# Kernel optimization log

Hardware: AMD Instinct MI355X
Metric: run time of the kernel (lower is better)

## Reference

```python
import jax, jax.numpy as jnp
import numpy as np

# Standard bitsandbytes NF4 codebook (16 values)
NF4_CODE = jnp.array([
    -1.0, -0.6961928009986877, -0.5250730514526367, -0.39491748809814453,
    -0.28444138169288635, -0.18477343022823334, -0.09105003625154495, 0.0,
    0.07958029955625534, 0.16093020141124725, 0.24611230194568634,
    0.33791524171829224, 0.44070982933044434, 0.5626170039176941,
    0.7229568362236023, 1.0], dtype=jnp.float32)

BLOCKSIZE = 64
IN_FEATURES = 4096
OUT_FEATURES = 11008


def setup_inputs() -> dict:
    key = jax.random.key(0)
    k1, k2, k3, k4 = jax.random.split(key, 4)
    x = jax.random.normal(k1, (4, 2048, IN_FEATURES), dtype=jnp.float32)
    weight_q = jax.random.randint(k2, (OUT_FEATURES, IN_FEATURES), 0, 16, dtype=jnp.int32)
    absmax = jax.random.uniform(k3, (OUT_FEATURES, IN_FEATURES // BLOCKSIZE), dtype=jnp.float32)
    bias = jax.random.normal(k4, (OUT_FEATURES,), dtype=jnp.float32)
    return {"x": x, "weight_q": weight_q, "absmax": absmax, "bias": bias}


def reference(x, weight_q, absmax, bias):
    out_f, in_f = weight_q.shape
    # Blockwise NF4 dequantization: code lookup * per-block absmax scale
    w_code = NF4_CODE[weight_q]                                   # [O, I]
    w_blocks = w_code.reshape(out_f, in_f // BLOCKSIZE, BLOCKSIZE)
    w = (w_blocks * absmax[:, :, None]).reshape(out_f, in_f)      # [O, I]
    # Linear: y = x @ W^T + b
    y = jnp.einsum('bsi,oi->bso', x, w) + bias
    return y
```

## Files before the change

### kernel.cpp

```cpp
#include <hip/hip_runtime.h>
#include <hip/hip_bf16.h>
#include <stdint.h>

typedef __attribute__((ext_vector_type(8))) short short8;
typedef __attribute__((ext_vector_type(8))) unsigned short ushort8;
typedef __attribute__((ext_vector_type(4))) float f32x4;

#define K_DIM 4096
#define N_DIM 11008
#define M_DIM 8192
#define BM 256
#define BN 256
#define BK 64
#define TILES (K_DIM / BK)

__constant__ float c_nf4[16] = {
    -1.0f, -0.6961928009986877f, -0.5250730514526367f, -0.39491748809814453f,
    -0.28444138169288635f, -0.18477343022823334f, -0.09105003625154495f, 0.0f,
    0.07958029955625534f, 0.16093020141124725f, 0.24611230194568634f,
    0.33791524171829224f, 0.44070982933044434f, 0.5626170039176941f,
    0.7229568362236023f, 1.0f};

__device__ __forceinline__ unsigned short f2bf(float f) {
    uint32_t u = __float_as_uint(f);
    u += 0x7fffu + ((u >> 16) & 1u);
    return (unsigned short)(u >> 16);
}

__global__ __launch_bounds__(256) void nf4_dequant_w(const int* __restrict__ q,
                                                     const float* __restrict__ absmax,
                                                     unsigned short* __restrict__ w) {
    __shared__ float lut[16];
    if (threadIdx.x < 16) lut[threadIdx.x] = c_nf4[threadIdx.x];
    __syncthreads();
    size_t t = (size_t)blockIdx.x * 256 + threadIdx.x;
    const int4* q4 = (const int4*)q;
    int4 qa = q4[2 * t];
    int4 qb = q4[2 * t + 1];
    float s = absmax[t >> 3];
    ushort8 o;
    o[0] = f2bf(lut[qa.x & 15] * s);
    o[1] = f2bf(lut[qa.y & 15] * s);
    o[2] = f2bf(lut[qa.z & 15] * s);
    o[3] = f2bf(lut[qa.w & 15] * s);
    o[4] = f2bf(lut[qb.x & 15] * s);
    o[5] = f2bf(lut[qb.y & 15] * s);
    o[6] = f2bf(lut[qb.z & 15] * s);
    o[7] = f2bf(lut[qb.w & 15] * s);
    ((ushort8*)w)[t] = o;
}

__global__ __launch_bounds__(256) void x_to_bf16(const float* __restrict__ x,
                                                 unsigned short* __restrict__ xb) {
    size_t t = (size_t)blockIdx.x * 256 + threadIdx.x;
    const float4* x4 = (const float4*)x;
    float4 a = x4[2 * t];
    float4 b = x4[2 * t + 1];
    ushort8 o;
    o[0] = f2bf(a.x); o[1] = f2bf(a.y); o[2] = f2bf(a.z); o[3] = f2bf(a.w);
    o[4] = f2bf(b.x); o[5] = f2bf(b.y); o[6] = f2bf(b.z); o[7] = f2bf(b.w);
    ((ushort8*)xb)[t] = o;
}

#define STAGE_HALF(gbase, lds_half, row0, k0)                                 \
  do {                                                                        \
    _Pragma("unroll")                                                         \
    for (int _g = 0; _g < 2; ++_g) {                                          \
      const int _i = _g * 512 + tid;                        \
      const int _r = _i >> 3;                           \
      const int _c = (_i & 7) ^ (_r & 7);                   \
      __builtin_amdgcn_global_load_lds(                                       \
          (const __attribute__((address_space(1))) void*)((gbase) +           \
              (size_t)((row0) + _r) * K_DIM + (k0) + _c * 8),                 \
          (__attribute__((address_space(3))) void*)((lds_half) +              \
              (_g * 512 + wave * 64) * 8),                                    \
          16, 0, 0);                                                          \
    }                                                                         \
  } while (0)

#define DS_A4(dst, rbase, X)                                                  \
  dst[0] = *(const short8*)(Ah + ((rbase) +  0) * 64 + (roff ^ (X)));         \
  dst[1] = *(const short8*)(Ah + ((rbase) + 16) * 64 + (roff ^ (X)));         \
  dst[2] = *(const short8*)(Ah + ((rbase) + 32) * 64 + (roff ^ (X)));         \
  dst[3] = *(const short8*)(Ah + ((rbase) + 48) * 64 + (roff ^ (X)));

#define DS_B4(dst, X)                                                         \
  dst[0] = *(const short8*)(Bh + (bbase +  0) * 64 + (roff ^ (X)));           \
  dst[1] = *(const short8*)(Bh + (bbase + 16) * 64 + (roff ^ (X)));           \
  dst[2] = *(const short8*)(Bh + (bbase + 32) * 64 + (roff ^ (X)));           \
  dst[3] = *(const short8*)(Bh + (bbase + 48) * 64 + (roff ^ (X)));

#define MFMA16(MI0, Ar, Br)                                                   \
  __builtin_amdgcn_s_setprio(1);                                              \
  do {                                                                        \
    _Pragma("unroll")                                                         \
    for (int _m = 0; _m < 4; ++_m) {                                          \
      _Pragma("unroll")                                                       \
      for (int _n = 0; _n < 4; ++_n)                                          \
        acc[(MI0) + _m][_n] = __builtin_amdgcn_mfma_f32_16x16x32_bf16(        \
            Ar[_m], Br[_n], acc[(MI0) + _m][_n], 0, 0, 0);                    \
    }                                                                         \
  } while (0);                                                                \
  __builtin_amdgcn_s_setprio(0);

__global__ __launch_bounds__(512, 2) void gemm256(const unsigned short* __restrict__ A,
                                                  const unsigned short* __restrict__ B,
                                                  const float* __restrict__ bias,
                                                  float* __restrict__ C) {
    __shared__ unsigned short As[2][2][128 * 64];
    __shared__ unsigned short Bs[2][2][128 * 64];

    const int tid  = threadIdx.x;
    const int wave = tid >> 6;
    const int lane = tid & 63;
    const int wm = wave >> 2;
    const int wn = wave & 3;
    const int lr = lane & 15;
    const int q  = lane >> 4;
    const int roff = lr * 64 + ((q ^ (lr & 7)) << 3);
    const int bbase = (wn & 1) * 64;

    const int nbn = N_DIM / BN;
    const int cpx = (int)gridDim.x >> 3;
    const int bid = (int)blockIdx.x;
    const int swz = (bid & 7) * cpx + (bid >> 3);
    const int bm = swz / nbn;
    const int bn = swz % nbn;

    const unsigned short* Ab = A + (size_t)bm * BM * K_DIM;
    const unsigned short* Bb = B + (size_t)bn * BN * K_DIM;

    f32x4 acc[8][4];
#pragma unroll
    for (int i = 0; i < 8; ++i)
#pragma unroll
        for (int j = 0; j < 4; ++j)
#pragma unroll
            for (int v = 0; v < 4; ++v) acc[i][j][v] = 0.0f;

    STAGE_HALF(Ab, &As[0][0][0], 0,   0); STAGE_HALF(Bb, &Bs[0][0][0], 0,   0);
    STAGE_HALF(Ab, &As[0][1][0], 128, 0); STAGE_HALF(Bb, &Bs[0][1][0], 128, 0);
    asm volatile("s_waitcnt vmcnt(0)" ::: "memory");
    asm volatile("s_barrier" ::: "memory");

    short8 aA[4], aB[4], aC[4], aD[4], bE[4], bO[4];

#pragma unroll 1
    for (int t = 0; t < TILES; ++t) {
        const int p = t & 1;
        int t1 = t + 1; if (t1 >= TILES) t1 = 0;
        const int k1 = t1 * BK;
        const unsigned short* Ah = &As[p][wm][0];
        const unsigned short* Bh = &Bs[p][wn >> 1][0];

        DS_A4(aA, 0, 0);
        DS_B4(bE, 0);
        DS_A4(aB, 64, 0);

        STAGE_HALF(Ab, &As[p ^ 1][0][0], 0,   k1);
        STAGE_HALF(Bb, &Bs[p ^ 1][0][0], 0,   k1);
        STAGE_HALF(Ab, &As[p ^ 1][1][0], 128, k1);
        STAGE_HALF(Bb, &Bs[p ^ 1][1][0], 128, k1);

        MFMA16(0, aA, bE);

        DS_B4(bO, 32);
        DS_A4(aC, 0, 32);

        MFMA16(4, aB, bE);

        DS_A4(aD, 64, 32);

        MFMA16(0, aC, bO);
        MFMA16(4, aD, bO);

        asm volatile("s_waitcnt lgkmcnt(0)" ::: "memory");
        __builtin_amdgcn_sched_barrier(0);
        asm volatile("s_waitcnt vmcnt(0)" ::: "memory");
        asm volatile("s_barrier" ::: "memory");
    }

    const int row0 = bm * BM + wm * 128 + (q << 2);
    const int col0 = bn * BN + wn * 64 + lr;
#pragma unroll
    for (int ni = 0; ni < 4; ++ni) {
        const int col = col0 + ni * 16;
        const float bv = bias[col];
#pragma unroll
        for (int mi = 0; mi < 8; ++mi) {
#pragma unroll
            for (int v = 0; v < 4; ++v) {
                C[(size_t)(row0 + mi * 16 + v) * N_DIM + col] = acc[mi][ni][v] + bv;
            }
        }
    }
}

extern "C" void kernel_launch(void* const* d_in, const int* in_sizes, int n_in,
                              void* d_out, int out_size, void* d_ws, size_t ws_size,
                              hipStream_t stream) {
    const float* x    = (const float*)d_in[0];
    const int*   wq   = (const int*)d_in[1];
    const float* am   = (const float*)d_in[2];
    const float* bias = (const float*)d_in[3];
    float* out = (float*)d_out;

    const size_t w_elems = (size_t)N_DIM * K_DIM;
    const size_t x_elems = (size_t)M_DIM * K_DIM;
    const size_t need = (w_elems + x_elems) * sizeof(unsigned short);
    if (ws_size < need) return;

    unsigned short* wbf = (unsigned short*)d_ws;
    unsigned short* xbf = wbf + w_elems;

    nf4_dequant_w<<<(int)(w_elems / 8 / 256), 256, 0, stream>>>(wq, am, wbf);
    x_to_bf16<<<(int)(x_elems / 8 / 256), 256, 0, stream>>>(x, xbf);

    const int grid = (M_DIM / BM) * (N_DIM / BN);
    gemm256<<<grid, 512, 0, stream>>>(xbf, wbf, bias, out);
}
```

Baseline: 815.7 us.

## Shrink GEMM tile to 256x128x32 with 4 waves and simpler LDS layout

```diff
diff --git a/kernel.cpp b/kernel.cpp
--- a/kernel.cpp
+++ b/kernel.cpp
@@ -10,8 +10,8 @@
 #define N_DIM 11008
 #define M_DIM 8192
 #define BM 256
-#define BN 256
-#define BK 64
+#define BN 128
+#define BK 32
 #define TILES (K_DIM / BK)
 
 __constant__ float c_nf4[16] = {
@@ -62,63 +62,47 @@
     ((ushort8*)xb)[t] = o;
 }
 
-#define STAGE_HALF(gbase, lds_half, row0, k0)                                 \
+#define STAGE(gbase, lds_sub, NG, k0)                                         \
   do {                                                                        \
     _Pragma("unroll")                                                         \
-    for (int _g = 0; _g < 2; ++_g) {                                          \
-      const int _i = _g * 512 + tid;                        \
-      const int _r = _i >> 3;                           \
-      const int _c = (_i & 7) ^ (_r & 7);                   \
+    for (int _g = 0; _g < NG; ++_g) {                                         \
+      const int _i = _g * 256 + tid;                         \
+      const int _r = _i >> 2;                                        \
+      const int _c = (_i & 3) << 3;                   \
       __builtin_amdgcn_global_load_lds(                                       \
           (const __attribute__((address_space(1))) void*)((gbase) +           \
-              (size_t)((row0) + _r) * K_DIM + (k0) + _c * 8),                 \
-          (__attribute__((address_space(3))) void*)((lds_half) +              \
-              (_g * 512 + wave * 64) * 8),                                    \
+              (size_t)_r * K_DIM + (k0) + _c),                                \
+          (__attribute__((address_space(3))) void*)((lds_sub) +               \
+              (_g * 256 + wave * 64) * 8),                                    \
           16, 0, 0);                                                          \
     }                                                                         \
   } while (0)
 
-#define DS_A4(dst, rbase, X)                                                  \
-  dst[0] = *(const short8*)(Ah + ((rbase) +  0) * 64 + (roff ^ (X)));         \
-  dst[1] = *(const short8*)(Ah + ((rbase) + 16) * 64 + (roff ^ (X)));         \
-  dst[2] = *(const short8*)(Ah + ((rbase) + 32) * 64 + (roff ^ (X)));         \
-  dst[3] = *(const short8*)(Ah + ((rbase) + 48) * 64 + (roff ^ (X)));
-
-#define DS_B4(dst, X)                                                         \
-  dst[0] = *(const short8*)(Bh + (bbase +  0) * 64 + (roff ^ (X)));           \
-  dst[1] = *(const short8*)(Bh + (bbase + 16) * 64 + (roff ^ (X)));           \
-  dst[2] = *(const short8*)(Bh + (bbase + 32) * 64 + (roff ^ (X)));           \
-  dst[3] = *(const short8*)(Bh + (bbase + 48) * 64 + (roff ^ (X)));
-
-#define MFMA16(MI0, Ar, Br)                                                   \
-  __builtin_amdgcn_s_setprio(1);                                              \
+#define MFMA32                                                                \
   do {                                                                        \
     _Pragma("unroll")                                                         \
-    for (int _m = 0; _m < 4; ++_m) {                                          \
+    for (int _m = 0; _m < 8; ++_m) {                                          \
       _Pragma("unroll")                                                       \
       for (int _n = 0; _n < 4; ++_n)                                          \
-        acc[(MI0) + _m][_n] = __builtin_amdgcn_mfma_f32_16x16x32_bf16(        \
-            Ar[_m], Br[_n], acc[(MI0) + _m][_n], 0, 0, 0);                    \
+        acc[_m][_n] = __builtin_amdgcn_mfma_f32_16x16x32_bf16(                \
+            af[_m], bfr[_n], acc[_m][_n], 0, 0, 0);                           \
     }                                                                         \
-  } while (0);                                                                \
-  __builtin_amdgcn_s_setprio(0);
+  } while (0)
 
-__global__ __launch_bounds__(512, 2) void gemm256(const unsigned short* __restrict__ A,
+__global__ __launch_bounds__(256, 2) void gemm256(const unsigned short* __restrict__ A,
                                                   const unsigned short* __restrict__ B,
                                                   const float* __restrict__ bias,
                                                   float* __restrict__ C) {
-    __shared__ unsigned short As[2][2][128 * 64];
-    __shared__ unsigned short Bs[2][2][128 * 64];
+    __shared__ unsigned short As[2][BM * 32];
+    __shared__ unsigned short Bs[2][BN * 32];
 
     const int tid  = threadIdx.x;
     const int wave = tid >> 6;
     const int lane = tid & 63;
-    const int wm = wave >> 2;
-    const int wn = wave & 3;
+    const int wm = wave >> 1;
+    const int wn = wave & 1;
     const int lr = lane & 15;
-    const int q  = lane >> 4;
-    const int roff = lr * 64 + ((q ^ (lr & 7)) << 3);
-    const int bbase = (wn & 1) * 64;
+    const int q8 = (lane >> 4) << 3;
 
     const int nbn = N_DIM / BN;
     const int cpx = (int)gridDim.x >> 3;
@@ -138,49 +122,43 @@
 #pragma unroll
             for (int v = 0; v < 4; ++v) acc[i][j][v] = 0.0f;
 
-    STAGE_HALF(Ab, &As[0][0][0], 0,   0); STAGE_HALF(Bb, &Bs[0][0][0], 0,   0);
-    STAGE_HALF(Ab, &As[0][1][0], 128, 0); STAGE_HALF(Bb, &Bs[0][1][0], 128, 0);
+    STAGE(Ab, &As[0][0], 4, 0);
+    STAGE(Bb, &Bs[0][0], 2, 0);
     asm volatile("s_waitcnt vmcnt(0)" ::: "memory");
     asm volatile("s_barrier" ::: "memory");
 
-    short8 aA[4], aB[4], aC[4], aD[4], bE[4], bO[4];
+    short8 af[8], bfr[4];
 
 #pragma unroll 1
     for (int t = 0; t < TILES; ++t) {
         const int p = t & 1;
         int t1 = t + 1; if (t1 >= TILES) t1 = 0;
         const int k1 = t1 * BK;
-        const unsigned short* Ah = &As[p][wm][0];
-        const unsigned short* Bh = &Bs[p][wn >> 1][0];
+        const unsigned short* Ah = &As[p][0];
+        const unsigned short* Bh = &Bs[p][0];
 
-        DS_A4(aA, 0, 0);
-        DS_B4(bE, 0);
-        DS_A4(aB, 64, 0);
+        STAGE(Ab, &As[p ^ 1][0], 4, k1);
+        STAGE(Bb, &Bs[p ^ 1][0], 2, k1);
 
-        STAGE_HALF(Ab, &As[p ^ 1][0][0], 0,   k1);
-        STAGE_HALF(Bb, &Bs[p ^ 1][0][0], 0,   k1);
-        STAGE_HALF(Ab, &As[p ^ 1][1][0], 128, k1);
-        STAGE_HALF(Bb, &Bs[p ^ 1][1][0], 128, k1);
+#pragma unroll
+        for (int mi = 0; mi < 8; ++mi)
+            af[mi] = *(const short8*)(Ah + (wm * 128 + mi * 16 + lr) * 32 + q8);
+#pragma unroll
+        for (int ni = 0; ni < 4; ++ni)
+            bfr[ni] = *(const short8*)(Bh + (wn * 64 + ni * 16 + lr) * 32 + q8);
 
-        MFMA16(0, aA, bE);
-
-        DS_B4(bO, 32);
-        DS_A4(aC, 0, 32);
-
-        MFMA16(4, aB, bE);
-
-        DS_A4(aD, 64, 32);
-
-        MFMA16(0, aC, bO);
-        MFMA16(4, aD, bO);
+        __builtin_amdgcn_s_setprio(1);
+        MFMA32;
+        __builtin_amdgcn_s_setprio(0);
 
         asm volatile("s_waitcnt lgkmcnt(0)" ::: "memory");
         __builtin_amdgcn_sched_barrier(0);
         asm volatile("s_waitcnt vmcnt(0)" ::: "memory");
         asm volatile("s_barrier" ::: "memory");
     }
+    asm volatile("s_waitcnt vmcnt(0)" ::: "memory");
 
-    const int row0 = bm * BM + wm * 128 + (q << 2);
+    const int row0 = bm * BM + wm * 128 + ((lane >> 4) << 2);
     const int col0 = bn * BN + wn * 64 + lr;
 #pragma unroll
     for (int ni = 0; ni < 4; ++ni) {
@@ -217,5 +195,5 @@
     x_to_bf16<<<(int)(x_elems / 8 / 256), 256, 0, stream>>>(x, xbf);
 
     const int grid = (M_DIM / BM) * (N_DIM / BN);
-    gemm256<<<grid, 512, 0, stream>>>(xbf, wbf, bias, out);
+    gemm256<<<grid, 256, 0, stream>>>(xbf, wbf, bias, out);
 }
```

Result: slower. 1.001 ms (+22.7%).

## Switch GEMM inner loop to 32x32x16 bf16 MFMA with matching LDS fragment layout

Applied to the files above, without the earlier changes.

```diff
diff --git a/kernel.cpp b/kernel.cpp
--- a/kernel.cpp
+++ b/kernel.cpp
@@ -4,7 +4,7 @@
 
 typedef __attribute__((ext_vector_type(8))) short short8;
 typedef __attribute__((ext_vector_type(8))) unsigned short ushort8;
-typedef __attribute__((ext_vector_type(4))) float f32x4;
+typedef __attribute__((ext_vector_type(16))) float f32x16;
 
 #define K_DIM 4096
 #define N_DIM 11008
@@ -66,9 +66,9 @@
   do {                                                                        \
     _Pragma("unroll")                                                         \
     for (int _g = 0; _g < 2; ++_g) {                                          \
-      const int _i = _g * 512 + tid;                        \
-      const int _r = _i >> 3;                           \
-      const int _c = (_i & 7) ^ (_r & 7);                   \
+      const int _i = _g * 512 + tid;                                          \
+      const int _r = _i >> 3;                                                 \
+      const int _c = (_i & 7) ^ (_r & 7);                                     \
       __builtin_amdgcn_global_load_lds(                                       \
           (const __attribute__((address_space(1))) void*)((gbase) +           \
               (size_t)((row0) + _r) * K_DIM + (k0) + _c * 8),                 \
@@ -78,27 +78,42 @@
     }                                                                         \
   } while (0)
 
-#define DS_A4(dst, rbase, X)                                                  \
-  dst[0] = *(const short8*)(Ah + ((rbase) +  0) * 64 + (roff ^ (X)));         \
-  dst[1] = *(const short8*)(Ah + ((rbase) + 16) * 64 + (roff ^ (X)));         \
-  dst[2] = *(const short8*)(Ah + ((rbase) + 32) * 64 + (roff ^ (X)));         \
-  dst[3] = *(const short8*)(Ah + ((rbase) + 48) * 64 + (roff ^ (X)));
-
-#define DS_B4(dst, X)                                                         \
-  dst[0] = *(const short8*)(Bh + (bbase +  0) * 64 + (roff ^ (X)));           \
-  dst[1] = *(const short8*)(Bh + (bbase + 16) * 64 + (roff ^ (X)));           \
-  dst[2] = *(const short8*)(Bh + (bbase + 32) * 64 + (roff ^ (X)));           \
-  dst[3] = *(const short8*)(Bh + (bbase + 48) * 64 + (roff ^ (X)));
-
-#define MFMA16(MI0, Ar, Br)                                                   \
+#define DS_A2(dst, Ah, MB0)                                                   \
+  do {                                                                        \
+    _Pragma("unroll")                                                         \
+    for (int _m = 0; _m < 2; ++_m) {                                          \
+      const unsigned short* _p = (Ah) + ((MB0) + _m) * 2048 + arow;           \
+      dst[_m][0] = *(const short8*)(_p + ck0);                                \
+      dst[_m][1] = *(const short8*)(_p + ck1);                                \
+      dst[_m][2] = *(const short8*)(_p + ck2);                                \
+      dst[_m][3] = *(const short8*)(_p + ck3);                                \
+    }                                                                         \
+  } while (0)
+
+#define DS_B2(dst, Bh)                                                        \
+  do {                                                                        \
+    _Pragma("unroll")                                                         \
+    for (int _n = 0; _n < 2; ++_n) {                                          \
+      const unsigned short* _p = (Bh) + (lb + _n * 32) * 64 + arow;           \
+      dst[_n][0] = *(const short8*)(_p + ck0);                                \
+      dst[_n][1] = *(const short8*)(_p + ck1);                                \
+      dst[_n][2] = *(const short8*)(_p + ck2);                                \
+      dst[_n][3] = *(const short8*)(_p + ck3);                                \
+    }                                                                         \
+  } while (0)
+
+#define MFMAB(ACC0, Ar)                                                       \
   __builtin_amdgcn_s_setprio(1);                                              \
   do {                                                                        \
     _Pragma("unroll")                                                         \
-    for (int _m = 0; _m < 4; ++_m) {                                          \
+    for (int _k = 0; _k < 4; ++_k) {                                          \
       _Pragma("unroll")                                                       \
-      for (int _n = 0; _n < 4; ++_n)                                          \
-        acc[(MI0) + _m][_n] = __builtin_amdgcn_mfma_f32_16x16x32_bf16(        \
-            Ar[_m], Br[_n], acc[(MI0) + _m][_n], 0, 0, 0);                    \
+      for (int _m = 0; _m < 2; ++_m) {                                        \
+        _Pragma("unroll")                                                     \
+        for (int _n = 0; _n < 2; ++_n)                                        \
+          acc[(ACC0) + _m][_n] = __builtin_amdgcn_mfma_f32_32x32x16_bf16(     \
+              Ar[_m][_k], bb[_n][_k], acc[(ACC0) + _m][_n], 0, 0, 0);         \
+      }                                                                       \
     }                                                                         \
   } while (0);                                                                \
   __builtin_amdgcn_s_setprio(0);
@@ -115,10 +130,15 @@
     const int lane = tid & 63;
     const int wm = wave >> 2;
     const int wn = wave & 3;
-    const int lr = lane & 15;
-    const int q  = lane >> 4;
-    const int roff = lr * 64 + ((q ^ (lr & 7)) << 3);
-    const int bbase = (wn & 1) * 64;
+    const int lrow = lane & 31;
+    const int khi  = lane >> 5;
+    const int lb   = (wn & 1) * 64;
+    const int arow = lrow * 64;
+    const int lx = lane & 7;
+    const int ck0 = (((0 << 1) | khi) ^ lx) << 3;
+    const int ck1 = (((1 << 1) | khi) ^ lx) << 3;
+    const int ck2 = (((2 << 1) | khi) ^ lx) << 3;
+    const int ck3 = (((3 << 1) | khi) ^ lx) << 3;
 
     const int nbn = N_DIM / BN;
     const int cpx = (int)gridDim.x >> 3;
@@ -130,20 +150,20 @@
     const unsigned short* Ab = A + (size_t)bm * BM * K_DIM;
     const unsigned short* Bb = B + (size_t)bn * BN * K_DIM;
 
-    f32x4 acc[8][4];
-#pragma unroll
-    for (int i = 0; i < 8; ++i)
-#pragma unroll
-        for (int j = 0; j < 4; ++j)
-#pragma unroll
-            for (int v = 0; v < 4; ++v) acc[i][j][v] = 0.0f;
+    f32x16 acc[4][2];
+#pragma unroll
+    for (int i = 0; i < 4; ++i)
+#pragma unroll
+        for (int j = 0; j < 2; ++j)
+#pragma unroll
+            for (int v = 0; v < 16; ++v) acc[i][j][v] = 0.0f;
 
     STAGE_HALF(Ab, &As[0][0][0], 0,   0); STAGE_HALF(Bb, &Bs[0][0][0], 0,   0);
     STAGE_HALF(Ab, &As[0][1][0], 128, 0); STAGE_HALF(Bb, &Bs[0][1][0], 128, 0);
     asm volatile("s_waitcnt vmcnt(0)" ::: "memory");
     asm volatile("s_barrier" ::: "memory");
 
-    short8 aA[4], aB[4], aC[4], aD[4], bE[4], bO[4];
+    short8 aE[2][4], aO[2][4], bb[2][4];
 
 #pragma unroll 1
     for (int t = 0; t < TILES; ++t) {
@@ -153,44 +173,39 @@
         const unsigned short* Ah = &As[p][wm][0];
         const unsigned short* Bh = &Bs[p][wn >> 1][0];
 
-        DS_A4(aA, 0, 0);
-        DS_B4(bE, 0);
-        DS_A4(aB, 64, 0);
+        DS_B2(bb, Bh);
+        DS_A2(aE, Ah, 0);
 
         STAGE_HALF(Ab, &As[p ^ 1][0][0], 0,   k1);
         STAGE_HALF(Bb, &Bs[p ^ 1][0][0], 0,   k1);
         STAGE_HALF(Ab, &As[p ^ 1][1][0], 128, k1);
         STAGE_HALF(Bb, &Bs[p ^ 1][1][0], 128, k1);
 
-        MFMA16(0, aA, bE);
-
-        DS_B4(bO, 32);
-        DS_A4(aC, 0, 32);
-
-        MFMA16(4, aB, bE);
-
-        DS_A4(aD, 64, 32);
-
-        MFMA16(0, aC, bO);
-        MFMA16(4, aD, bO);
+        MFMAB(0, aE);
+
+        DS_A2(aO, Ah, 2);
+
+        MFMAB(2, aO);
 
         asm volatile("s_waitcnt lgkmcnt(0)" ::: "memory");
         __builtin_amdgcn_sched_barrier(0);
         asm volatile("s_waitcnt vmcnt(0)" ::: "memory");
         asm volatile("s_barrier" ::: "memory");
     }
-
-    const int row0 = bm * BM + wm * 128 + (q << 2);
-    const int col0 = bn * BN + wn * 64 + lr;
-#pragma unroll
-    for (int ni = 0; ni < 4; ++ni) {
-        const int col = col0 + ni * 16;
+    asm volatile("s_waitcnt vmcnt(0)" ::: "memory");
+
+    const int rbase = bm * BM + wm * 128 + 4 * khi;
+    const int col0 = bn * BN + wn * 64 + lrow;
+#pragma unroll
+    for (int nb = 0; nb < 2; ++nb) {
+        const int col = col0 + nb * 32;
         const float bv = bias[col];
 #pragma unroll
-        for (int mi = 0; mi < 8; ++mi) {
-#pragma unroll
-            for (int v = 0; v < 4; ++v) {
-                C[(size_t)(row0 + mi * 16 + v) * N_DIM + col] = acc[mi][ni][v] + bv;
+        for (int mb = 0; mb < 4; ++mb) {
+#pragma unroll
+            for (int r = 0; r < 16; ++r) {
+                const int row = rbase + mb * 32 + (r & 3) + 8 * (r >> 2);
+                C[(size_t)row * N_DIM + col] = acc[mb][nb][r] + bv;
             }
         }
     }
```

Result: no change. 828.4 us (+1.6%).
